# Optimization experiments

Measured on AMD Instinct MI355X. Metric: run time of the kernel, lower is better.

## Reference

```python
import jax, jax.numpy as jnp
import numpy as np
import math

FS = 44100.0
HOP = 256
N_BANDS = 24
KS_BUF = 768  # > max delay 44100/60 = 735 samples


def _lpc1(x, a):
    # order-1 all-pole (sample_wise_lpc with order 1, per-batch constant coeff):
    # y[n] = x[n] - a*y[n-1];  x: [B,N], a: [B]
    def step(yp, xt):
        y = xt - a * yp
        return y, y
    _, ys = jax.lax.scan(step, jnp.zeros_like(a), x.T)
    return ys.T


def _diff_ks(f0_frames, exc, l_b):
    # differentiable Karplus-Strong: fractional-delay loop + 2-tap damping filter.
    # f0_frames: [B,F] Hz, exc: [B,N], l_b: [B,F,2] (loop_coeff, loop_mix logits)
    B, N = exc.shape
    g = 0.999 * jax.nn.sigmoid(l_b[..., 0])   # loop gain in (0, 0.999)
    s = jax.nn.sigmoid(l_b[..., 1])           # loop-filter mix
    up = lambda p: jnp.repeat(p, HOP, axis=1)[:, :N]
    g_s, s_s = up(g), up(s)
    f0_s = up(jnp.clip(f0_frames, 60.0, None))
    D = jnp.clip(FS / f0_s, 2.0, 735.0)        # delay in samples
    Di = jnp.floor(D).astype(jnp.int32)
    fr = (D - Di).astype(exc.dtype)
    L = KS_BUF

    def step(carry, xs):
        buf, n = carry                         # buf: [B,L] circular delay line
        x_t, Di_t, fr_t, g_t, s_t = xs         # each [B]
        i1 = jnp.mod(n - Di_t, L)
        i2 = jnp.mod(n - Di_t - 1, L)
        i3 = jnp.mod(n - Di_t - 2, L)
        take = lambda i: jnp.take_along_axis(buf, i[:, None], axis=1)[:, 0]
        b1, b2, b3 = take(i1), take(i2), take(i3)
        z = (1.0 - fr_t) * b1 + fr_t * b2      # fractional-delay read y[n-D]
        z1 = (1.0 - fr_t) * b2 + fr_t * b3     # y[n-D-1]
        y = x_t + g_t * ((1.0 - s_t) * z + s_t * z1)
        buf = buf.at[:, jnp.mod(n, L)].set(y)
        return (buf, n + 1), y

    xs = (exc.T, Di.T, fr.T, g_s.T, s_s.T)
    init = (jnp.zeros((B, L), exc.dtype), jnp.int32(0))
    _, ys = jax.lax.scan(step, init, xs)
    return ys.T


def _body(x, body_gains):
    # bank of 24 two-pole resonators, log-spaced 80..8000 Hz, Q=10
    fc = jnp.geomspace(80.0, 8000.0, N_BANDS).astype(x.dtype)
    w = 2.0 * jnp.pi * fc / FS
    r = jnp.exp(-jnp.pi * fc / (10.0 * FS))
    a1 = -2.0 * r * jnp.cos(w)
    a2 = r * r
    b0 = 1.0 - r
    B = x.shape[0]

    def step(carry, xt):
        y1, y2 = carry                          # [B,24] each
        y = b0 * xt[:, None] - a1 * y1 - a2 * y2
        return (y, y1), jnp.sum(y * body_gains, axis=-1)

    init = (jnp.zeros((B, N_BANDS), x.dtype), jnp.zeros((B, N_BANDS), x.dtype))
    _, out = jax.lax.scan(step, init, x.T)
    return out.T


def _forward(excitation, pitch, w1, b1, w2, b2, excitation_gain, body_gains):
    B, _, N = excitation.shape
    h = jax.nn.relu(pitch @ w1.T + b1)
    mlp_out = h @ w2.T + b2                     # [B,3]
    loop_coeff = jnp.clip(mlp_out[:, 0], -2.0, 2.5)
    loop_mix = jnp.clip(mlp_out[:, 1], -2.5, 0.0)
    frames = N // HOP
    l_b = jnp.broadcast_to(jnp.stack([loop_coeff, loop_mix], -1)[:, None, :], (B, frames, 2))
    f0_frames = jnp.broadcast_to(pitch, (B, frames))
    exc_sq = (excitation * excitation_gain)[:, 0, :]
    f0_hz = jnp.clip(pitch[:, 0], 60.0, None)
    mult = jnp.clip(2.0 + 6.0 * (f0_hz - 60.0) / 600.0, 2.0, 8.0)
    cutoff = jnp.minimum(2.0 * jnp.pi * f0_hz * mult / FS, jnp.pi * 0.9)
    alpha = 1.0 - jnp.exp(-cutoff)
    exc_f = _lpc1(exc_sq * alpha[:, None], alpha - 1.0)   # pre-KS one-pole LP
    string = _diff_ks(f0_frames, exc_f, l_b)
    loop_post = jnp.clip(mlp_out[:, 2], -4.0, 4.0)
    cutoff_post = jnp.minimum(jnp.pi * jax.nn.sigmoid(loop_post), jnp.pi * 0.99)
    alpha_p = 1.0 - jnp.exp(-cutoff_post)
    string = _lpc1(string * alpha_p[:, None], alpha_p - 1.0)  # post one-pole LP
    out = _body(string, body_gains)
    return out[:, None, :], loop_coeff.mean(), loop_mix.mean(), loop_post.mean()


def setup_inputs():
    key = jax.random.key(0)
    k = jax.random.split(key, 6)
    B, N = 8, 32768
    excitation = jax.random.normal(k[0], (B, 1, N), dtype=jnp.float32)
    pitch = 60.0 + 600.0 * jax.random.uniform(k[1], (B, 1), dtype=jnp.float32)
    bnd1 = 0.1 * math.sqrt(6.0 / (1 + 16))   # xavier_uniform, gain 0.1
    bnd2 = 0.1 * math.sqrt(6.0 / (16 + 3))
    w1 = jax.random.uniform(k[2], (16, 1), jnp.float32, -bnd1, bnd1)
    b1 = jnp.zeros((16,), jnp.float32)
    w2 = jax.random.uniform(k[3], (3, 16), jnp.float32, -bnd2, bnd2)
    b2 = jnp.array([0.9, 0.0, 0.0], jnp.float32)
    excitation_gain = jnp.array(0.25, jnp.float32)
    body_gains = 0.006 * jnp.ones((1, N_BANDS), jnp.float32)
    return {"excitation": excitation, "pitch": pitch, "w1": w1, "b1": b1,
            "w2": w2, "b2": b2, "excitation_gain": excitation_gain,
            "body_gains": body_gains}


def reference(excitation, pitch, w1, b1, w2, b2, excitation_gain, body_gains):
    return _forward(excitation, pitch, w1, b1, w2, b2, excitation_gain, body_gains)
```

## Files before the change

### kernel.cpp

```cpp
#include <hip/hip_runtime.h>
#include <math.h>

#define NSAMP 32768
#define FS_F 44100.0f
#define PI_F 3.14159265358979323846f
#define T1 1024
#define FLAG_MAGIC 0x5A5A5A5A

#define XCAP 33536
#define LWS_OFF 33536
#define TABS_OFF 33568
#define SMEM_FLOATS 40480

struct BParams {
  float alpha, alpha_p;
  float fr, g, s;
  int Di;
  float lc, lm, lp;
};

__device__ inline float sigmoidf_(float x) { return 1.0f / (1.0f + expf(-x)); }

__device__ inline BParams compute_params(int b, const float* __restrict__ pitch,
                                         const float* __restrict__ w1,
                                         const float* __restrict__ b1,
                                         const float* __restrict__ w2,
                                         const float* __restrict__ b2) {
  BParams P;
  float p = pitch[b];
  float h[16];
#pragma unroll
  for (int i = 0; i < 16; ++i) {
    float v = fmaf(p, w1[i], b1[i]);
    h[i] = v > 0.0f ? v : 0.0f;
  }
  float m[3];
#pragma unroll
  for (int j = 0; j < 3; ++j) {
    float acc = b2[j];
#pragma unroll
    for (int i = 0; i < 16; ++i) acc = fmaf(h[i], w2[j * 16 + i], acc);
    m[j] = acc;
  }
  P.lc = fminf(fmaxf(m[0], -2.0f), 2.5f);
  P.lm = fminf(fmaxf(m[1], -2.5f), 0.0f);
  P.lp = fminf(fmaxf(m[2], -4.0f), 4.0f);
  P.g = 0.999f * sigmoidf_(P.lc);
  P.s = sigmoidf_(P.lm);
  float f0 = fmaxf(p, 60.0f);
  float D = fminf(fmaxf(FS_F / f0, 2.0f), 735.0f);
  int Di = (int)floorf(D);
  P.fr = D - (float)Di;
  P.Di = Di;
  float mult = fminf(fmaxf(2.0f + 6.0f * (f0 - 60.0f) / 600.0f, 2.0f), 8.0f);
  float cutoff = fminf(2.0f * PI_F * f0 * mult / FS_F, PI_F * 0.9f);
  P.alpha = 1.0f - expf(-cutoff);
  float cpost = fminf(PI_F * sigmoidf_(P.lp), PI_F * 0.99f);
  P.alpha_p = 1.0f - expf(-cpost);
  return P;
}

__device__ inline float rlv(float v, int l) {
  return __int_as_float(__builtin_amdgcn_readlane(__float_as_int(v), l));
}
__device__ inline float shr1(float v, float bnd) {
  return __int_as_float(__builtin_amdgcn_update_dpp(
      __float_as_int(bnd), __float_as_int(v), 0x138 , 0xf, 0xf,
      false));
}
__device__ inline float ror1(float v) {
  return __int_as_float(__builtin_amdgcn_update_dpp(
      __float_as_int(v), __float_as_int(v), 0x13C , 0xf, 0xf,
      false));
}

__device__ inline void band_coef(int k, float& a1, float& a2, float& b0) {
  float fc = 80.0f * exp2f((float)k * (6.64385618977472436f / 23.0f));
  float w = 2.0f * PI_F * fc / FS_F;
  float r = expf(-PI_F * fc / (10.0f * FS_F));
  a1 = -2.0f * r * cosf(w);
  a2 = r * r;
  b0 = 1.0f - r;
}

__device__ inline void gen_tables(float* __restrict__ tabs, int W) {
  if (W >= 120) return;
  const int j = W / 5, sub = W % 5;
  float A1, A2, B0;
  band_coef(j, A1, A2, B0);
  if (sub == 0) *(float4*)&tabs[j * 4] = make_float4(A1, A2, B0, 0.f);
  float Q00 = -A1, Q01 = -A2, Q10 = 1.f, Q11 = 0.f;
#pragma unroll
  for (int sq = 0; sq < 2; ++sq) {
    float n00 = fmaf(Q00, Q00, Q01 * Q10);
    float n01 = fmaf(Q00, Q01, Q01 * Q11);
    float n10 = fmaf(Q10, Q00, Q11 * Q10);
    float n11 = fmaf(Q10, Q01, Q11 * Q11);
    Q00 = n00; Q01 = n01; Q10 = n10; Q11 = n11;
  }
  float K00 = Q00, K01 = Q01, K10 = Q10, K11 = Q11;
#pragma unroll
  for (int sq = 0; sq < 2; ++sq) {
    float n00 = fmaf(Q00, Q00, Q01 * Q10);
    float n01 = fmaf(Q00, Q01, Q01 * Q11);
    float n10 = fmaf(Q10, Q00, Q11 * Q10);
    float n11 = fmaf(Q10, Q01, Q11 * Q11);
    Q00 = n00; Q01 = n01; Q10 = n10; Q11 = n11;
  }
  float L00[7], L01[7], L10[7], L11[7];
  L00[0] = fmaf(Q00, K00, Q01 * K10);
  L01[0] = fmaf(Q00, K01, Q01 * K11);
  L10[0] = fmaf(Q10, K00, Q11 * K10);
  L11[0] = fmaf(Q10, K01, Q11 * K11);
#pragma unroll
  for (int k = 0; k < 6; ++k) {
    float s00 = fmaf(L00[k], L00[k], L01[k] * L10[k]);
    float s01 = fmaf(L00[k], L01[k], L01[k] * L11[k]);
    float s10 = fmaf(L10[k], L00[k], L11[k] * L10[k]);
    float s11 = fmaf(L10[k], L01[k], L11[k] * L11[k]);
    L00[k + 1] = s00; L01[k + 1] = s01; L10[k + 1] = s10; L11[k + 1] = s11;
  }
  if (sub == 0) {
#pragma unroll
    for (int k = 0; k < 6; ++k)
      *(float4*)&tabs[96 + (k * 24 + j) * 4] =
          make_float4(L00[k], L01[k], L10[k], L11[k]);
    *(float4*)&tabs[672 + j * 4] = make_float4(L00[6], L01[6], L10[6], L11[6]);
  }
  int l0 = sub * 13, l1 = l0 + 13;
  if (l1 > 64) l1 = 64;
  for (int l = l0; l < l1; ++l) {
    float R00 = 1.f, R01 = 0.f, R10 = 0.f, R11 = 1.f;
#pragma unroll
    for (int bit = 0; bit < 6; ++bit) {
      if ((l >> bit) & 1) {
        float n00 = fmaf(L00[bit], R00, L01[bit] * R10);
        float n01 = fmaf(L00[bit], R01, L01[bit] * R11);
        float n10 = fmaf(L10[bit], R00, L11[bit] * R10);
        float n11 = fmaf(L10[bit], R01, L11[bit] * R11);
        R00 = n00; R01 = n01; R10 = n10; R11 = n11;
      }
    }
    *(float4*)&tabs[768 + (j * 64 + l) * 4] = make_float4(R00, R01, R10, R11);
  }
}

template <int KNUM>
__device__ void ks_wave0(float* __restrict__ yg, const float* xall, int lane,
                         int C, float c0w, float c1w, float c2w, int s1,
                         int n0, int end, int span) {
  const int lq1 = (C - 1) - (KNUM - 1) * 64;
  const int W = n0 - s1;
  float yp[KNUM], xC[KNUM], xN[KNUM];
  float p1 = 0.f, p2 = 0.f;
#pragma unroll
  for (int k = 0; k < KNUM; ++k) {
    yp[k] = 0.f;
    xC[k] = xall[lane + (k << 6)];
    xN[k] = xall[C + lane + (k << 6)];
  }
  int rel = 0;
  while (rel + C <= W) {
    float b2v[KNUM], b3v[KNUM];
    b2v[0] = shr1(yp[0], p1);
#pragma unroll
    for (int k = 1; k < KNUM; ++k) b2v[k] = shr1(yp[k], ror1(yp[k - 1]));
    b3v[0] = shr1(b2v[0], p2);
#pragma unroll
    for (int k = 1; k < KNUM; ++k) b3v[k] = shr1(b2v[k], ror1(b2v[k - 1]));
    float p1n = rlv(yp[KNUM - 1], lq1);
    float p2n = rlv(b2v[KNUM - 1], lq1);
#pragma unroll
    for (int k = 0; k < KNUM; ++k)
      yp[k] = fmaf(c0w, yp[k], fmaf(c2w, b3v[k], fmaf(c1w, b2v[k], xC[k])));
    p1 = p1n;
    p2 = p2n;
    int r2 = rel + 2 * C;
    if (r2 < span) {
      const float* xp = &xall[r2 + lane];
#pragma unroll
      for (int k = 0; k < KNUM; ++k) {
        xC[k] = xN[k];
        xN[k] = xp[k << 6];
      }
    } else {
#pragma unroll
      for (int k = 0; k < KNUM; ++k) xC[k] = xN[k];
    }
    rel += C;
  }
  while (rel < span) {
    float b2v[KNUM], b3v[KNUM];
    b2v[0] = shr1(yp[0], p1);
#pragma unroll
    for (int k = 1; k < KNUM; ++k) b2v[k] = shr1(yp[k], ror1(yp[k - 1]));
    b3v[0] = shr1(b2v[0], p2);
#pragma unroll
    for (int k = 1; k < KNUM; ++k) b3v[k] = shr1(b2v[k], ror1(b2v[k - 1]));
    float p1n = rlv(yp[KNUM - 1], lq1);
    float p2n = rlv(b2v[KNUM - 1], lq1);
#pragma unroll
    for (int k = 0; k < KNUM; ++k)
      yp[k] = fmaf(c0w, yp[k], fmaf(c2w, b3v[k], fmaf(c1w, b2v[k], xC[k])));
    p1 = p1n;
    p2 = p2n;
#pragma unroll
    for (int k = 0; k < KNUM; ++k) {
      int i = lane + (k << 6);
      int n = s1 + rel + i;
      bool okl = (k < KNUM - 1) || (lane <= lq1);
      if (okl && n >= n0 && n < end) yg[n] = yp[k];
    }
    int r2 = rel + 2 * C;
    if (r2 < span) {
      const float* xp = &xall[r2 + lane];
#pragma unroll
      for (int k = 0; k < KNUM; ++k) {
        xC[k] = xN[k];
        xN[k] = xp[k << 6];
      }
    } else {
#pragma unroll
      for (int k = 0; k < KNUM; ++k) xC[k] = xN[k];
    }
    rel += C;
  }
}

__device__ inline void ks_phase(int b, int q, const BParams& P,
                                const float* __restrict__ exc, float scale0,
                                float* __restrict__ buf1, float* xall,
                                float* lws, float* tabs, int t) {
  const int C = P.Di;
  const int n0 = q << 10;
  float lg = -logf(P.g);
  int Wp = (int)ceilf(10.5f / fmaxf(lg, 1e-6f));
  if (Wp > 64) Wp = 64;
  if (Wp < 4) Wp = 4;
  int W = Wp * C;
  if (W > n0) W = n0;
  W = (W + 3) & ~3;
  const int s1 = n0 - W;
  const int span = W + T1;
  const int end = n0 + T1;
  const int NSG = (span + 2047) >> 11;
  float* yg = buf1 + (size_t)b * NSAMP;
  const float* xg = exc + (size_t)b * NSAMP;

  const float c = 1.0f - P.alpha;
  const float scale = scale0 * P.alpha;
  const float c2v = c * c, c4 = c2v * c2v, c8 = c4 * c4, c16 = c8 * c8;
  const float c32 = c16 * c16, c64 = c32 * c32, c128 = c64 * c64;
  const float c256 = c128 * c128, c512 = c256 * c256, c1024 = c512 * c512;
  const float c2048 = c1024 * c1024;
  const int lane = t & 63, wid = t >> 6;
  const float c32lane = exp2f((float)(lane << 5) * log2f(c));

  for (int r = 0; r < 5; ++r) {
    int si = r * 4 + wid;
    if (si > NSG) break;
    int sg = si - 1;
    int gbase = s1 + (sg << 11) + (lane << 5);
    float4 pf[8];
#pragma unroll
    for (int i = 0; i < 8; ++i) {
      int g = gbase + 4 * i;
      float4 v = make_float4(0.f, 0.f, 0.f, 0.f);
      if (g >= 0 && g + 3 < NSAMP) v = *(const float4*)&xg[g];
      pf[i] = v;
    }
    float S = 0.0f;
#pragma unroll
    for (int i = 0; i < 8; ++i) {
      S = fmaf(c, S, scale * pf[i].x);
      S = fmaf(c, S, scale * pf[i].y);
      S = fmaf(c, S, scale * pf[i].z);
      S = fmaf(c, S, scale * pf[i].w);
    }
    float Sw = S, u;
    u = __shfl_up(Sw, 1);  if (lane >= 1)  Sw = fmaf(c32, u, Sw);
    u = __shfl_up(Sw, 2);  if (lane >= 2)  Sw = fmaf(c64, u, Sw);
    u = __shfl_up(Sw, 4);  if (lane >= 4)  Sw = fmaf(c128, u, Sw);
    u = __shfl_up(Sw, 8);  if (lane >= 8)  Sw = fmaf(c256, u, Sw);
    u = __shfl_up(Sw, 16); if (lane >= 16) Sw = fmaf(c512, u, Sw);
    u = __shfl_up(Sw, 32); if (lane >= 32) Sw = fmaf(c1024, u, Sw);
    float tot = rlv(Sw, 63);
    float Sex = __shfl_up(Sw, 1);
    if (lane == 0) Sex = 0.0f;
    if (lane == 0) lws[si] = tot;
    if (sg >= 0) {
      float v = Sex;
#pragma unroll
      for (int i = 0; i < 8; ++i) {
        float4 y;
        v = fmaf(c, v, scale * pf[i].x); y.x = v;
        v = fmaf(c, v, scale * pf[i].y); y.y = v;
        v = fmaf(c, v, scale * pf[i].z); y.z = v;
        v = fmaf(c, v, scale * pf[i].w); y.w = v;
        pf[i] = y;
      }
      int o = (sg << 11) + (lane << 5);
#pragma unroll
      for (int i = 0; i < 8; ++i) {
        int ci = (lane + i) & 7;
        *(float4*)&xall[o + 4 * ci] = pf[ci];
      }
    }
  }
  if (4 * t < 768) {
    *(float4*)&xall[(NSG << 11) + 4 * t] = make_float4(0.f, 0.f, 0.f, 0.f);
  }
  __syncthreads();
  {
    float p4[8];
    p4[0] = 1.0f;
#pragma unroll
    for (int i = 1; i < 8; ++i) p4[i] = p4[i - 1] * c4;
    for (int r = 0; r < 5; ++r) {
      int si = r * 4 + wid;
      if (si > NSG) break;
      int sg = si - 1;
      if (sg < 0) continue;
      float vr = 0.0f;
      for (int i = 0; i < si; ++i) vr = fmaf(c2048, vr, lws[i]);
      float corr0 = c * (c32lane * vr);
      int o = (sg << 11) + (lane << 5);
#pragma unroll
      for (int i = 0; i < 8; ++i) {
        int ci = (lane + i) & 7;
        float4 y = *(float4*)&xall[o + 4 * ci];
        float f = corr0 * p4[ci];
        y.x += f; f *= c;
        y.y += f; f *= c;
        y.z += f; f *= c;
        y.w += f;
        *(float4*)&xall[o + 4 * ci] = y;
      }
    }
  }
  __syncthreads();

  const float c0w = P.g * (1.0f - P.s) * (1.0f - P.fr);
  const float c1w = P.g * ((1.0f - P.s) * P.fr + P.s * (1.0f - P.fr));
  const float c2w = P.g * P.s * P.fr;
  if (wid == 0) {
    switch ((C + 63) >> 6) {
      case 2:  ks_wave0<2>(yg, xall, lane, C, c0w, c1w, c2w, s1, n0, end, span); break;
      case 3:  ks_wave0<3>(yg, xall, lane, C, c0w, c1w, c2w, s1, n0, end, span); break;
      case 4:  ks_wave0<4>(yg, xall, lane, C, c0w, c1w, c2w, s1, n0, end, span); break;
      case 5:  ks_wave0<5>(yg, xall, lane, C, c0w, c1w, c2w, s1, n0, end, span); break;
      case 6:  ks_wave0<6>(yg, xall, lane, C, c0w, c1w, c2w, s1, n0, end, span); break;
      case 7:  ks_wave0<7>(yg, xall, lane, C, c0w, c1w, c2w, s1, n0, end, span); break;
      case 8:  ks_wave0<8>(yg, xall, lane, C, c0w, c1w, c2w, s1, n0, end, span); break;
      case 9:  ks_wave0<9>(yg, xall, lane, C, c0w, c1w, c2w, s1, n0, end, span); break;
      case 10: ks_wave0<10>(yg, xall, lane, C, c0w, c1w, c2w, s1, n0, end, span); break;
      case 11: ks_wave0<11>(yg, xall, lane, C, c0w, c1w, c2w, s1, n0, end, span); break;
      default: ks_wave0<12>(yg, xall, lane, C, c0w, c1w, c2w, s1, n0, end, span); break;
    }
  } else if (wid >= 2) {
    gen_tables(tabs, (wid - 2) * 64 + lane);
  }
}

__device__ inline void lpc_lds(const float* __restrict__ xg,
                               float* __restrict__ sl, int s2, int nt, int lim,
                               float scale, float c, int t, float* lws) {
  const int lane = t & 63, wid = t >> 6;
  float c2v = c * c, c4 = c2v * c2v, c8 = c4 * c4;
  float m1 = c8, m2 = m1 * m1, m4 = m2 * m2, m8 = m4 * m4, m16 = m8 * m8,
        m32 = m16 * m16;
  float c512 = m32 * m32;
  float c2048 = c512 * c512;
  c2048 *= c2048;
  float l2c = log2f(c);
  float c8lane = exp2f((float)(8 * lane) * l2c);
  float cgk = exp2f((float)(8 * t) * l2c);
  float vrun = 0.0f;
  for (int tile = 0; tile < nt; ++tile) {
    __syncthreads();
    int g0 = s2 + (tile << 11) + 8 * t;
    float4 xa = make_float4(0.f, 0.f, 0.f, 0.f);
    float4 xb = make_float4(0.f, 0.f, 0.f, 0.f);
    if (g0 + 3 < lim) xa = *(const float4*)&xg[g0];
    if (g0 + 7 < lim) xb = *(const float4*)&xg[g0 + 4];
    float S = 0.0f;
    S = fmaf(c, S, scale * xa.x); S = fmaf(c, S, scale * xa.y);
    S = fmaf(c, S, scale * xa.z); S = fmaf(c, S, scale * xa.w);
    S = fmaf(c, S, scale * xb.x); S = fmaf(c, S, scale * xb.y);
    S = fmaf(c, S, scale * xb.z); S = fmaf(c, S, scale * xb.w);
    float Sw = S, u;
    u = __shfl_up(Sw, 1);  if (lane >= 1)  Sw = fmaf(m1, u, Sw);
    u = __shfl_up(Sw, 2);  if (lane >= 2)  Sw = fmaf(m2, u, Sw);
    u = __shfl_up(Sw, 4);  if (lane >= 4)  Sw = fmaf(m4, u, Sw);
    u = __shfl_up(Sw, 8);  if (lane >= 8)  Sw = fmaf(m8, u, Sw);
    u = __shfl_up(Sw, 16); if (lane >= 16) Sw = fmaf(m16, u, Sw);
    u = __shfl_up(Sw, 32); if (lane >= 32) Sw = fmaf(m32, u, Sw);
    if (lane == 63) lws[wid] = Sw;
    __syncthreads();
    float a0 = lws[0], a1w = lws[1], a2w = lws[2], a3w = lws[3];
    float carry = (wid == 1)   ? a0
                  : (wid == 2) ? fmaf(c512, a0, a1w)
                  : (wid == 3) ? fmaf(c512, fmaf(c512, a0, a1w), a2w)
                               : 0.0f;
    float Sprev = __shfl_up(Sw, 1);
    float Sex = (lane == 0) ? 0.0f : Sprev;
    Sex = fmaf(c8lane, carry, Sex);
    float v = fmaf(cgk, vrun, Sex);
    int o = g0 - s2;
    float4 ya, yb;
    v = fmaf(c, v, scale * xa.x); ya.x = v;
    v = fmaf(c, v, scale * xa.y); ya.y = v;
    v = fmaf(c, v, scale * xa.z); ya.z = v;
    v = fmaf(c, v, scale * xa.w); ya.w = v;
    v = fmaf(c, v, scale * xb.x); yb.x = v;
    v = fmaf(c, v, scale * xb.y); yb.y = v;
    v = fmaf(c, v, scale * xb.z); yb.z = v;
    v = fmaf(c, v, scale * xb.w); yb.w = v;
    *(float4*)&sl[o] = ya;
    *(float4*)&sl[o + 4] = yb;
    float tS = fmaf(c512, fmaf(c512, fmaf(c512, a0, a1w), a2w), a3w);
    vrun = fmaf(c2048, vrun, tS);
  }
}

__device__ inline void body_phase(int b, int q, const BParams& P,
                                  const float* __restrict__ gains,
                                  const float* __restrict__ buf1,
                                  float* __restrict__ out, float* sl,
                                  float* lws, float (*lc0)[8],
                                  float (*lc1)[8], const float* tabs, int t) {
  const int lane = t & 63, wid = t >> 6;
  const int n0 = q << 10;
  const int base = n0 - 4096;
  int s2 = base - 256;
  if (s2 < 0) s2 = 0;
  const int end = n0 + 1024;
  const int nt = (end - s2 + 2047) >> 11;

  lpc_lds(buf1 + (size_t)b * NSAMP, sl, s2, nt, end, P.alpha_p,
          1.0f - P.alpha_p, t, lws);
  __syncthreads();

  const float* bandcL = tabs;
  const float* QlevL = tabs + 96;
  const float* QwL = tabs + 672;
  const float* RtabL = tabs + 768;

  const int tb = base + 20 * t;
  float4 acc[5];
#pragma unroll
  for (int i = 0; i < 5; ++i) acc[i] = make_float4(0.f, 0.f, 0.f, 0.f);

  for (int g = 0; g < 3; ++g) {
    float A1[8], A2[8], B0[8], GN[8];
#pragma unroll
    for (int j = 0; j < 8; ++j) {
      int k = g * 8 + j;
      float4 bc = *(const float4*)&bandcL[k * 4];
      A1[j] = bc.x; A2[j] = bc.y; B0[j] = bc.z;
      GN[j] = gains[k];
    }
    float cv0[8], cv1[8];
#pragma unroll
    for (int j = 0; j < 8; ++j) cv0[j] = cv1[j] = 0.f;
    for (int i = 0; i < 5; ++i) {
      int n = tb + 4 * i;
      float4 xv = make_float4(0.f, 0.f, 0.f, 0.f);
      if (n >= 0) xv = *(const float4*)&sl[n - s2];
#pragma unroll
      for (int e = 0; e < 4; ++e) {
        float xi = e == 0 ? xv.x : e == 1 ? xv.y : e == 2 ? xv.z : xv.w;
#pragma unroll
        for (int j = 0; j < 8; ++j) {
          float nc = fmaf(B0[j], xi, -fmaf(A1[j], cv0[j], A2[j] * cv1[j]));
          cv1[j] = cv0[j];
          cv0[j] = nc;
        }
      }
    }
    int kl = 0;
    for (int off = 1; off <= 32; off <<= 1, ++kl) {
      float q00[8], q01[8], q10[8], q11[8];
#pragma unroll
      for (int j = 0; j < 8; ++j) {
        float4 qv = *(const float4*)&QlevL[(kl * 24 + g * 8 + j) * 4];
        q00[j] = qv.x; q01[j] = qv.y; q10[j] = qv.z; q11[j] = qv.w;
      }
#pragma unroll
      for (int j = 0; j < 8; ++j) {
        float u0 = __shfl_up(cv0[j], off);
        float u1 = __shfl_up(cv1[j], off);
        if (lane >= off) {
          float nc0 = fmaf(q00[j], u0, fmaf(q01[j], u1, cv0[j]));
          float nc1 = fmaf(q10[j], u0, fmaf(q11[j], u1, cv1[j]));
          cv0[j] = nc0;
          cv1[j] = nc1;
        }
      }
    }
    __syncthreads();
    if (lane == 63) {
#pragma unroll
      for (int j = 0; j < 8; ++j) {
        lc0[wid][j] = cv0[j];
        lc1[wid][j] = cv1[j];
      }
    }
    __syncthreads();
    float qw00[8], qw01[8], qw10[8], qw11[8];
#pragma unroll
    for (int j = 0; j < 8; ++j) {
      float4 qv = *(const float4*)&QwL[(g * 8 + j) * 4];
      qw00[j] = qv.x; qw01[j] = qv.y; qw10[j] = qv.z; qw11[j] = qv.w;
    }
    float car0[8], car1[8];
#pragma unroll
    for (int j = 0; j < 8; ++j) car0[j] = car1[j] = 0.f;
    for (int v = 0; v < wid; ++v) {
#pragma unroll
      for (int j = 0; j < 8; ++j) {
        float n0c = fmaf(qw00[j], car0[j], fmaf(qw01[j], car1[j], lc0[v][j]));
        float n1c = fmaf(qw10[j], car0[j], fmaf(qw11[j], car1[j], lc1[v][j]));
        car0[j] = n0c;
        car1[j] = n1c;
      }
    }
    float y1[8], y2[8];
#pragma unroll
    for (int j = 0; j < 8; ++j) {
      float4 rv = *(const float4*)&RtabL[((g * 8 + j) * 64 + lane) * 4];
      float e0 = __shfl_up(cv0[j], 1);
      float e1 = __shfl_up(cv1[j], 1);
      if (lane == 0) { e0 = 0.f; e1 = 0.f; }
      y1[j] = fmaf(rv.x, car0[j], fmaf(rv.y, car1[j], e0));
      y2[j] = fmaf(rv.z, car0[j], fmaf(rv.w, car1[j], e1));
    }
    if (tb + 20 > n0) {
      for (int i = 0; i < 5; ++i) {
        float4 xv = *(const float4*)&sl[tb - s2 + 4 * i];
        float4 ov = acc[i];
#pragma unroll
        for (int e = 0; e < 4; ++e) {
          float xi = e == 0 ? xv.x : e == 1 ? xv.y : e == 2 ? xv.z : xv.w;
          float a = 0.f;
#pragma unroll
          for (int j = 0; j < 8; ++j) {
            float yv = fmaf(B0[j], xi, -fmaf(A1[j], y1[j], A2[j] * y2[j]));
            y2[j] = y1[j];
            y1[j] = yv;
            a = fmaf(GN[j], yv, a);
          }
          if (e == 0) ov.x += a;
          else if (e == 1) ov.y += a;
          else if (e == 2) ov.z += a;
          else ov.w += a;
        }
        acc[i] = ov;
      }
    }
  }
  if (tb + 20 > n0) {
    float* outb = out + (size_t)b * NSAMP;
#pragma unroll
    for (int i = 0; i < 5; ++i) {
      int n = tb + 4 * i;
      if (n >= n0) *(float4*)&outb[n] = acc[i];
    }
  }
}

__global__ void __launch_bounds__(256, 1) synth_all(
    const float* __restrict__ exc, const float* __restrict__ pitch,
    const float* __restrict__ w1, const float* __restrict__ b1,
    const float* __restrict__ w2, const float* __restrict__ b2,
    const float* __restrict__ eg, const float* __restrict__ gains,
    float* __restrict__ buf1, int* __restrict__ flags,
    float* __restrict__ out) {
  extern __shared__ float smem[];
  const int blk = blockIdx.x;
  const int b = blk >> 5, q = blk & 31;
  const int t = threadIdx.x;

  BParams P = compute_params(b, pitch, w1, b1, w2, b2);
  if (blk == 0 && t < 64) {
    int bb = (t < 8) ? t : 0;
    BParams Q = compute_params(bb, pitch, w1, b1, w2, b2);
    float slc = 0.f, slm = 0.f, slp = 0.f;
    for (int i = 0; i < 8; ++i) {
      slc += rlv(Q.lc, i);
      slm += rlv(Q.lm, i);
      slp += rlv(Q.lp, i);
    }
    if (t == 0) {
      out[8 * NSAMP + 0] = slc / 8.0f;
      out[8 * NSAMP + 1] = slm / 8.0f;
      out[8 * NSAMP + 2] = slp / 8.0f;
    }
  }

  ks_phase(b, q, P, exc, eg[0], buf1, smem, smem + LWS_OFF, smem + TABS_OFF, t);
  __syncthreads();

  const int n0 = q << 10;
  int s2 = n0 - 4096 - 256;
  if (s2 < 0) s2 = 0;
  const int qlo = s2 >> 10;
  if (t == 0) {
    __hip_atomic_store(&flags[blk], FLAG_MAGIC, __ATOMIC_RELEASE,
                       __HIP_MEMORY_SCOPE_AGENT);
    for (int f = qlo; f < q; ++f) {
      while (__hip_atomic_load(&flags[b * 32 + f], __ATOMIC_ACQUIRE,
                               __HIP_MEMORY_SCOPE_AGENT) != FLAG_MAGIC) {
        __builtin_amdgcn_s_sleep(8);
      }
    }
  }
  __syncthreads();

  body_phase(b, q, P, gains, buf1, out, smem, smem + 6144,
             (float(*)[8])(smem + 6152), (float(*)[8])(smem + 6184),
             smem + TABS_OFF, t);
}

extern "C" void kernel_launch(void* const* d_in, const int* in_sizes, int n_in,
                              void* d_out, int out_size, void* d_ws, size_t ws_size,
                              hipStream_t stream) {
  const float* exc = (const float*)d_in[0];
  const float* pitch = (const float*)d_in[1];
  const float* w1 = (const float*)d_in[2];
  const float* b1 = (const float*)d_in[3];
  const float* w2 = (const float*)d_in[4];
  const float* b2 = (const float*)d_in[5];
  const float* eg = (const float*)d_in[6];
  const float* bg = (const float*)d_in[7];
  float* out = (float*)d_out;
  float* buf1 = (float*)d_ws;
  int* flags = (int*)(buf1 + 8 * NSAMP);

  static int lds_set = 0;
  if (!lds_set) {
    hipFuncSetAttribute(reinterpret_cast<const void*>(synth_all),
                        hipFuncAttributeMaxDynamicSharedMemorySize,
                        SMEM_FLOATS * 4);
    lds_set = 1;
  }
  hipLaunchKernelGGL(synth_all, dim3(256), dim3(256), SMEM_FLOATS * 4, stream,
                     exc, pitch, w1, b1, w2, b2, eg, bg, buf1, flags, out);
}
```

Baseline: 126.7 us.

## Restructure excitation prefilter scan into block-wide per-segment scan with prefetch

Replaces the two-pass segment scan (each wave scans a 2048-sample segment with 32 samples per lane, then a second pass applies carry corrections) with a sequential loop over segments. In that loop all 256 threads cooperatively scan each segment at 8 samples per thread, combine wave totals through LDS and carry a running value, so no correction pass is needed. Global loads for the next segment are double-buffered in registers. The trade is two barriers per segment and a serialized segment loop, in exchange for dropping the second LDS read-modify-write pass and cutting per-thread serial work.

```diff
diff --git a/kernel.cpp b/kernel.cpp
--- a/kernel.cpp
+++ b/kernel.cpp
@@ -74,6 +74,10 @@
       false));
 }
 
+__device__ inline void barrier_lgkm() {
+  asm volatile("s_waitcnt lgkmcnt(0)\n\ts_barrier" ::: "memory");
+}
+
 __device__ inline void band_coef(int k, float& a1, float& a2, float& b0) {
   float fc = 80.0f * exp2f((float)k * (6.64385618977472436f / 23.0f));
   float w = 2.0f * PI_F * fc / FS_F;
@@ -143,6 +147,67 @@
     }
     *(float4*)&tabs[768 + (j * 64 + l) * 4] = make_float4(R00, R01, R10, R11);
   }
+}
+
+struct SCtx {
+  float scale, c;
+  float m1, m2, m4, m8, m16, m32, c512, c2048, c8lane, cgk;
+  float vrun;
+  float* lws;
+};
+
+__device__ inline void ld2(const float* __restrict__ p, int g0, float4& a,
+                           float4& b) {
+  a = make_float4(0.f, 0.f, 0.f, 0.f);
+  b = make_float4(0.f, 0.f, 0.f, 0.f);
+  if (g0 >= 0 && g0 + 3 < NSAMP) a = *(const float4*)&p[g0];
+  if (g0 + 4 >= 0 && g0 + 7 < NSAMP) b = *(const float4*)&p[g0 + 4];
+}
+
+__device__ inline void scan_seg_flat(SCtx& SC, float* xall, int sg, bool write,
+                                     int t, float4 xa, float4 xb) {
+  const int lane = t & 63, wid = t >> 6;
+  barrier_lgkm();
+  const float c = SC.c, scale = SC.scale;
+  float S = 0.0f;
+  S = fmaf(c, S, scale * xa.x); S = fmaf(c, S, scale * xa.y);
+  S = fmaf(c, S, scale * xa.z); S = fmaf(c, S, scale * xa.w);
+  S = fmaf(c, S, scale * xb.x); S = fmaf(c, S, scale * xb.y);
+  S = fmaf(c, S, scale * xb.z); S = fmaf(c, S, scale * xb.w);
+  float Sw = S, u;
+  u = __shfl_up(Sw, 1);  if (lane >= 1)  Sw = fmaf(SC.m1, u, Sw);
+  u = __shfl_up(Sw, 2);  if (lane >= 2)  Sw = fmaf(SC.m2, u, Sw);
+  u = __shfl_up(Sw, 4);  if (lane >= 4)  Sw = fmaf(SC.m4, u, Sw);
+  u = __shfl_up(Sw, 8);  if (lane >= 8)  Sw = fmaf(SC.m8, u, Sw);
+  u = __shfl_up(Sw, 16); if (lane >= 16) Sw = fmaf(SC.m16, u, Sw);
+  u = __shfl_up(Sw, 32); if (lane >= 32) Sw = fmaf(SC.m32, u, Sw);
+  if (lane == 63) SC.lws[wid] = Sw;
+  barrier_lgkm();
+  float a0 = SC.lws[0], a1w = SC.lws[1], a2w = SC.lws[2], a3w = SC.lws[3];
+  float carry = (wid == 1)   ? a0
+                : (wid == 2) ? fmaf(SC.c512, a0, a1w)
+                : (wid == 3) ? fmaf(SC.c512, fmaf(SC.c512, a0, a1w), a2w)
+                             : 0.0f;
+  float Sprev = __shfl_up(Sw, 1);
+  float Sex = (lane == 0) ? 0.0f : Sprev;
+  Sex = fmaf(SC.c8lane, carry, Sex);
+  float v = fmaf(SC.cgk, SC.vrun, Sex);
+  float4 ya, yb;
+  v = fmaf(c, v, scale * xa.x); ya.x = v;
+  v = fmaf(c, v, scale * xa.y); ya.y = v;
+  v = fmaf(c, v, scale * xa.z); ya.z = v;
+  v = fmaf(c, v, scale * xa.w); ya.w = v;
+  v = fmaf(c, v, scale * xb.x); yb.x = v;
+  v = fmaf(c, v, scale * xb.y); yb.y = v;
+  v = fmaf(c, v, scale * xb.z); yb.z = v;
+  v = fmaf(c, v, scale * xb.w); yb.w = v;
+  if (write) {
+    int o = (sg << 11) + 8 * t;
+    *(float4*)&xall[o] = ya;
+    *(float4*)&xall[o + 4] = yb;
+  }
+  float tS = fmaf(SC.c512, fmaf(SC.c512, fmaf(SC.c512, a0, a1w), a2w), a3w);
+  SC.vrun = fmaf(SC.c2048, SC.vrun, tS);
 }
 
 template <int KNUM>
@@ -247,102 +312,47 @@
   float* yg = buf1 + (size_t)b * NSAMP;
   const float* xg = exc + (size_t)b * NSAMP;
 
-  const float c = 1.0f - P.alpha;
-  const float scale = scale0 * P.alpha;
-  const float c2v = c * c, c4 = c2v * c2v, c8 = c4 * c4, c16 = c8 * c8;
-  const float c32 = c16 * c16, c64 = c32 * c32, c128 = c64 * c64;
-  const float c256 = c128 * c128, c512 = c256 * c256, c1024 = c512 * c512;
-  const float c2048 = c1024 * c1024;
-  const int lane = t & 63, wid = t >> 6;
-  const float c32lane = exp2f((float)(lane << 5) * log2f(c));
-
-  for (int r = 0; r < 5; ++r) {
-    int si = r * 4 + wid;
-    if (si > NSG) break;
-    int sg = si - 1;
-    int gbase = s1 + (sg << 11) + (lane << 5);
-    float4 pf[8];
-#pragma unroll
-    for (int i = 0; i < 8; ++i) {
-      int g = gbase + 4 * i;
-      float4 v = make_float4(0.f, 0.f, 0.f, 0.f);
-      if (g >= 0 && g + 3 < NSAMP) v = *(const float4*)&xg[g];
-      pf[i] = v;
-    }
-    float S = 0.0f;
-#pragma unroll
-    for (int i = 0; i < 8; ++i) {
-      S = fmaf(c, S, scale * pf[i].x);
-      S = fmaf(c, S, scale * pf[i].y);
-      S = fmaf(c, S, scale * pf[i].z);
-      S = fmaf(c, S, scale * pf[i].w);
-    }
-    float Sw = S, u;
-    u = __shfl_up(Sw, 1);  if (lane >= 1)  Sw = fmaf(c32, u, Sw);
-    u = __shfl_up(Sw, 2);  if (lane >= 2)  Sw = fmaf(c64, u, Sw);
-    u = __shfl_up(Sw, 4);  if (lane >= 4)  Sw = fmaf(c128, u, Sw);
-    u = __shfl_up(Sw, 8);  if (lane >= 8)  Sw = fmaf(c256, u, Sw);
-    u = __shfl_up(Sw, 16); if (lane >= 16) Sw = fmaf(c512, u, Sw);
-    u = __shfl_up(Sw, 32); if (lane >= 32) Sw = fmaf(c1024, u, Sw);
-    float tot = rlv(Sw, 63);
-    float Sex = __shfl_up(Sw, 1);
-    if (lane == 0) Sex = 0.0f;
-    if (lane == 0) lws[si] = tot;
-    if (sg >= 0) {
-      float v = Sex;
-#pragma unroll
-      for (int i = 0; i < 8; ++i) {
-        float4 y;
-        v = fmaf(c, v, scale * pf[i].x); y.x = v;
-        v = fmaf(c, v, scale * pf[i].y); y.y = v;
-        v = fmaf(c, v, scale * pf[i].z); y.z = v;
-        v = fmaf(c, v, scale * pf[i].w); y.w = v;
-        pf[i] = y;
-      }
-      int o = (sg << 11) + (lane << 5);
-#pragma unroll
-      for (int i = 0; i < 8; ++i) {
-        int ci = (lane + i) & 7;
-        *(float4*)&xall[o + 4 * ci] = pf[ci];
-      }
-    }
+  SCtx SC;
+  SC.c = 1.0f - P.alpha;
+  SC.scale = scale0 * P.alpha;
+  {
+    float c = SC.c;
+    float c2v = c * c, c4 = c2v * c2v, c8 = c4 * c4;
+    SC.m1 = c8;
+    SC.m2 = SC.m1 * SC.m1;
+    SC.m4 = SC.m2 * SC.m2;
+    SC.m8 = SC.m4 * SC.m4;
+    SC.m16 = SC.m8 * SC.m8;
+    SC.m32 = SC.m16 * SC.m16;
+    SC.c512 = SC.m32 * SC.m32;
+    float c1024 = SC.c512 * SC.c512;
+    SC.c2048 = c1024 * c1024;
+    float l2c = log2f(c);
+    SC.c8lane = exp2f((float)(8 * (t & 63)) * l2c);
+    SC.cgk = exp2f((float)(8 * t) * l2c);
+  }
+  SC.vrun = 0.0f;
+  SC.lws = lws;
+
+  float4 xa, xb, na, nb;
+  float4 ta = make_float4(0.f, 0.f, 0.f, 0.f);
+  float4 tb = make_float4(0.f, 0.f, 0.f, 0.f);
+  ld2(xg, s1 - 2048 + 8 * t, xa, xb);
+  ld2(xg, s1 + 8 * t, na, nb);
+  for (int si = 0; si <= NSG; ++si) {
+    if (si + 2 <= NSG) ld2(xg, s1 + ((si + 1) << 11) + 8 * t, ta, tb);
+    scan_seg_flat(SC, xall, si - 1, si > 0, t, xa, xb);
+    xa = na; xb = nb; na = ta; nb = tb;
   }
   if (4 * t < 768) {
     *(float4*)&xall[(NSG << 11) + 4 * t] = make_float4(0.f, 0.f, 0.f, 0.f);
-  }
-  __syncthreads();
-  {
-    float p4[8];
-    p4[0] = 1.0f;
-#pragma unroll
-    for (int i = 1; i < 8; ++i) p4[i] = p4[i - 1] * c4;
-    for (int r = 0; r < 5; ++r) {
-      int si = r * 4 + wid;
-      if (si > NSG) break;
-      int sg = si - 1;
-      if (sg < 0) continue;
-      float vr = 0.0f;
-      for (int i = 0; i < si; ++i) vr = fmaf(c2048, vr, lws[i]);
-      float corr0 = c * (c32lane * vr);
-      int o = (sg << 11) + (lane << 5);
-#pragma unroll
-      for (int i = 0; i < 8; ++i) {
-        int ci = (lane + i) & 7;
-        float4 y = *(float4*)&xall[o + 4 * ci];
-        float f = corr0 * p4[ci];
-        y.x += f; f *= c;
-        y.y += f; f *= c;
-        y.z += f; f *= c;
-        y.w += f;
-        *(float4*)&xall[o + 4 * ci] = y;
-      }
-    }
   }
   __syncthreads();
 
   const float c0w = P.g * (1.0f - P.s) * (1.0f - P.fr);
   const float c1w = P.g * ((1.0f - P.s) * P.fr + P.s * (1.0f - P.fr));
   const float c2w = P.g * P.s * P.fr;
+  const int lane = t & 63, wid = t >> 6;
   if (wid == 0) {
     switch ((C + 63) >> 6) {
       case 2:  ks_wave0<2>(yg, xall, lane, C, c0w, c1w, c2w, s1, n0, end, span); break;
```

Measured after the change: 110.7 us. 1.14x faster.

## Pipeline excitation LPC prefilter in wave 1 with KS recurrence via progress flag

Applied to the files above, without the earlier changes.

The block-parallel LPC prefilter of the excitation, which used all four waves, two block barriers and a separate correction pass, is replaced. One wave now computes the prefilter segment by segment with a running carry and double-buffered global loads, and publishes progress through an LDS atomic counter. The Karplus-Strong wave polls that counter and starts consuming segments while later ones are still being produced. This removes the barriers and the correction pass and overlaps the prefilter with the serial recurrence, at the cost of serialising the prefilter onto a single wave and adding spin-wait polling.

```diff
diff --git a/kernel.cpp b/kernel.cpp
--- a/kernel.cpp
+++ b/kernel.cpp
@@ -7,10 +7,10 @@
 #define T1 1024
 #define FLAG_MAGIC 0x5A5A5A5A
 
-#define XCAP 33536
-#define LWS_OFF 33536
-#define TABS_OFF 33568
-#define SMEM_FLOATS 40480
+#define XALL_FLOATS 33792
+#define PROG_OFF 33792
+#define TABS_OFF 33808
+#define SMEM_FLOATS 40720
 
 struct BParams {
   float alpha, alpha_p;
@@ -145,92 +145,119 @@
   }
 }
 
+__device__ inline void w1_load(const float* __restrict__ xg, int s1, int seg,
+                               int lane, float4* pf) {
+  const int base = s1 + (seg << 11) + (lane << 5);
+#pragma unroll
+  for (int i = 0; i < 8; ++i) {
+    const int g = base + 4 * i;
+    float4 v = make_float4(0.f, 0.f, 0.f, 0.f);
+    if (g >= 0 && g + 3 < NSAMP) v = *(const float4*)&xg[g];
+    pf[i] = v;
+  }
+}
+
 template <int KNUM>
-__device__ void ks_wave0(float* __restrict__ yg, const float* xall, int lane,
-                         int C, float c0w, float c1w, float c2w, int s1,
-                         int n0, int end, int span) {
+__device__ void ks_wave0(float* __restrict__ yg, const float* xall,
+                         int* __restrict__ prog, int lane, int C, float c0w,
+                         float c1w, float c2w, int s1, int n0, int end,
+                         int span, int NSG) {
   const int lq1 = (C - 1) - (KNUM - 1) * 64;
   const int W = n0 - s1;
   float yp[KNUM], xC[KNUM], xN[KNUM];
   float p1 = 0.f, p2 = 0.f;
-#pragma unroll
-  for (int k = 0; k < KNUM; ++k) {
-    yp[k] = 0.f;
-    xC[k] = xall[lane + (k << 6)];
-    xN[k] = xall[C + lane + (k << 6)];
-  }
   int rel = 0;
-  while (rel + C <= W) {
-    float b2v[KNUM], b3v[KNUM];
-    b2v[0] = shr1(yp[0], p1);
-#pragma unroll
-    for (int k = 1; k < KNUM; ++k) b2v[k] = shr1(yp[k], ror1(yp[k - 1]));
-    b3v[0] = shr1(b2v[0], p2);
-#pragma unroll
-    for (int k = 1; k < KNUM; ++k) b3v[k] = shr1(b2v[k], ror1(b2v[k - 1]));
-    float p1n = rlv(yp[KNUM - 1], lq1);
-    float p2n = rlv(b2v[KNUM - 1], lq1);
-#pragma unroll
-    for (int k = 0; k < KNUM; ++k)
-      yp[k] = fmaf(c0w, yp[k], fmaf(c2w, b3v[k], fmaf(c1w, b2v[k], xC[k])));
-    p1 = p1n;
-    p2 = p2n;
-    int r2 = rel + 2 * C;
-    if (r2 < span) {
-      const float* xp = &xall[r2 + lane];
+#pragma unroll
+  for (int k = 0; k < KNUM; ++k) { yp[k] = 0.f; xC[k] = 0.f; xN[k] = 0.f; }
+  for (int s = 0; s < NSG; ++s) {
+    int need = s + 3;
+    if (need > NSG) need = NSG;
+    while (__hip_atomic_load(prog, __ATOMIC_ACQUIRE,
+                             __HIP_MEMORY_SCOPE_WORKGROUP) < need) {
+      __builtin_amdgcn_s_sleep(1);
+    }
+    if (s == 0) {
 #pragma unroll
       for (int k = 0; k < KNUM; ++k) {
-        xC[k] = xN[k];
-        xN[k] = xp[k << 6];
-      }
-    } else {
-#pragma unroll
-      for (int k = 0; k < KNUM; ++k) xC[k] = xN[k];
-    }
-    rel += C;
-  }
-  while (rel < span) {
-    float b2v[KNUM], b3v[KNUM];
-    b2v[0] = shr1(yp[0], p1);
-#pragma unroll
-    for (int k = 1; k < KNUM; ++k) b2v[k] = shr1(yp[k], ror1(yp[k - 1]));
-    b3v[0] = shr1(b2v[0], p2);
-#pragma unroll
-    for (int k = 1; k < KNUM; ++k) b3v[k] = shr1(b2v[k], ror1(b2v[k - 1]));
-    float p1n = rlv(yp[KNUM - 1], lq1);
-    float p2n = rlv(b2v[KNUM - 1], lq1);
-#pragma unroll
-    for (int k = 0; k < KNUM; ++k)
-      yp[k] = fmaf(c0w, yp[k], fmaf(c2w, b3v[k], fmaf(c1w, b2v[k], xC[k])));
-    p1 = p1n;
-    p2 = p2n;
-#pragma unroll
-    for (int k = 0; k < KNUM; ++k) {
-      int i = lane + (k << 6);
-      int n = s1 + rel + i;
-      bool okl = (k < KNUM - 1) || (lane <= lq1);
-      if (okl && n >= n0 && n < end) yg[n] = yp[k];
-    }
-    int r2 = rel + 2 * C;
-    if (r2 < span) {
-      const float* xp = &xall[r2 + lane];
+        int i = lane + (k << 6);
+        xC[k] = xall[i];
+        xN[k] = xall[C + i];
+      }
+    }
+    int fence = (s + 1) << 11;
+    if (fence > span) fence = span;
+    while (rel + C <= W && rel < fence) {
+      float b2v[KNUM], b3v[KNUM];
+      b2v[0] = shr1(yp[0], p1);
+#pragma unroll
+      for (int k = 1; k < KNUM; ++k) b2v[k] = shr1(yp[k], ror1(yp[k - 1]));
+      b3v[0] = shr1(b2v[0], p2);
+#pragma unroll
+      for (int k = 1; k < KNUM; ++k) b3v[k] = shr1(b2v[k], ror1(b2v[k - 1]));
+      float p1n = rlv(yp[KNUM - 1], lq1);
+      float p2n = rlv(b2v[KNUM - 1], lq1);
+#pragma unroll
+      for (int k = 0; k < KNUM; ++k)
+        yp[k] = fmaf(c0w, yp[k], fmaf(c2w, b3v[k], fmaf(c1w, b2v[k], xC[k])));
+      p1 = p1n;
+      p2 = p2n;
+      int r2 = rel + 2 * C;
+      if (r2 < span) {
+        const float* xp = &xall[r2 + lane];
+#pragma unroll
+        for (int k = 0; k < KNUM; ++k) {
+          xC[k] = xN[k];
+          xN[k] = xp[k << 6];
+        }
+      } else {
+#pragma unroll
+        for (int k = 0; k < KNUM; ++k) xC[k] = xN[k];
+      }
+      rel += C;
+    }
+    while (rel < fence) {
+      float b2v[KNUM], b3v[KNUM];
+      b2v[0] = shr1(yp[0], p1);
+#pragma unroll
+      for (int k = 1; k < KNUM; ++k) b2v[k] = shr1(yp[k], ror1(yp[k - 1]));
+      b3v[0] = shr1(b2v[0], p2);
+#pragma unroll
+      for (int k = 1; k < KNUM; ++k) b3v[k] = shr1(b2v[k], ror1(b2v[k - 1]));
+      float p1n = rlv(yp[KNUM - 1], lq1);
+      float p2n = rlv(b2v[KNUM - 1], lq1);
+#pragma unroll
+      for (int k = 0; k < KNUM; ++k)
+        yp[k] = fmaf(c0w, yp[k], fmaf(c2w, b3v[k], fmaf(c1w, b2v[k], xC[k])));
+      p1 = p1n;
+      p2 = p2n;
 #pragma unroll
       for (int k = 0; k < KNUM; ++k) {
-        xC[k] = xN[k];
-        xN[k] = xp[k << 6];
-      }
-    } else {
-#pragma unroll
-      for (int k = 0; k < KNUM; ++k) xC[k] = xN[k];
-    }
-    rel += C;
+        int i = lane + (k << 6);
+        int n = s1 + rel + i;
+        bool okl = (k < KNUM - 1) || (lane <= lq1);
+        if (okl && n >= n0 && n < end) yg[n] = yp[k];
+      }
+      int r2 = rel + 2 * C;
+      if (r2 < span) {
+        const float* xp = &xall[r2 + lane];
+#pragma unroll
+        for (int k = 0; k < KNUM; ++k) {
+          xC[k] = xN[k];
+          xN[k] = xp[k << 6];
+        }
+      } else {
+#pragma unroll
+        for (int k = 0; k < KNUM; ++k) xC[k] = xN[k];
+      }
+      rel += C;
+    }
   }
 }
 
 __device__ inline void ks_phase(int b, int q, const BParams& P,
                                 const float* __restrict__ exc, float scale0,
                                 float* __restrict__ buf1, float* xall,
-                                float* lws, float* tabs, int t) {
+                                int* prog, float* tabs, int t) {
   const int C = P.Di;
   const int n0 = q << 10;
   float lg = -logf(P.g);
@@ -249,115 +276,86 @@
 
   const float c = 1.0f - P.alpha;
   const float scale = scale0 * P.alpha;
-  const float c2v = c * c, c4 = c2v * c2v, c8 = c4 * c4, c16 = c8 * c8;
-  const float c32 = c16 * c16, c64 = c32 * c32, c128 = c64 * c64;
-  const float c256 = c128 * c128, c512 = c256 * c256, c1024 = c512 * c512;
-  const float c2048 = c1024 * c1024;
   const int lane = t & 63, wid = t >> 6;
-  const float c32lane = exp2f((float)(lane << 5) * log2f(c));
-
-  for (int r = 0; r < 5; ++r) {
-    int si = r * 4 + wid;
-    if (si > NSG) break;
-    int sg = si - 1;
-    int gbase = s1 + (sg << 11) + (lane << 5);
-    float4 pf[8];
-#pragma unroll
-    for (int i = 0; i < 8; ++i) {
-      int g = gbase + 4 * i;
-      float4 v = make_float4(0.f, 0.f, 0.f, 0.f);
-      if (g >= 0 && g + 3 < NSAMP) v = *(const float4*)&xg[g];
-      pf[i] = v;
-    }
-    float S = 0.0f;
-#pragma unroll
-    for (int i = 0; i < 8; ++i) {
-      S = fmaf(c, S, scale * pf[i].x);
-      S = fmaf(c, S, scale * pf[i].y);
-      S = fmaf(c, S, scale * pf[i].z);
-      S = fmaf(c, S, scale * pf[i].w);
-    }
-    float Sw = S, u;
-    u = __shfl_up(Sw, 1);  if (lane >= 1)  Sw = fmaf(c32, u, Sw);
-    u = __shfl_up(Sw, 2);  if (lane >= 2)  Sw = fmaf(c64, u, Sw);
-    u = __shfl_up(Sw, 4);  if (lane >= 4)  Sw = fmaf(c128, u, Sw);
-    u = __shfl_up(Sw, 8);  if (lane >= 8)  Sw = fmaf(c256, u, Sw);
-    u = __shfl_up(Sw, 16); if (lane >= 16) Sw = fmaf(c512, u, Sw);
-    u = __shfl_up(Sw, 32); if (lane >= 32) Sw = fmaf(c1024, u, Sw);
-    float tot = rlv(Sw, 63);
-    float Sex = __shfl_up(Sw, 1);
-    if (lane == 0) Sex = 0.0f;
-    if (lane == 0) lws[si] = tot;
-    if (sg >= 0) {
-      float v = Sex;
-#pragma unroll
-      for (int i = 0; i < 8; ++i) {
-        float4 y;
-        v = fmaf(c, v, scale * pf[i].x); y.x = v;
-        v = fmaf(c, v, scale * pf[i].y); y.y = v;
-        v = fmaf(c, v, scale * pf[i].z); y.z = v;
-        v = fmaf(c, v, scale * pf[i].w); y.w = v;
-        pf[i] = y;
-      }
-      int o = (sg << 11) + (lane << 5);
-#pragma unroll
-      for (int i = 0; i < 8; ++i) {
-        int ci = (lane + i) & 7;
-        *(float4*)&xall[o + 4 * ci] = pf[ci];
-      }
-    }
-  }
-  if (4 * t < 768) {
-    *(float4*)&xall[(NSG << 11) + 4 * t] = make_float4(0.f, 0.f, 0.f, 0.f);
-  }
-  __syncthreads();
-  {
-    float p4[8];
-    p4[0] = 1.0f;
-#pragma unroll
-    for (int i = 1; i < 8; ++i) p4[i] = p4[i - 1] * c4;
-    for (int r = 0; r < 5; ++r) {
-      int si = r * 4 + wid;
-      if (si > NSG) break;
-      int sg = si - 1;
-      if (sg < 0) continue;
-      float vr = 0.0f;
-      for (int i = 0; i < si; ++i) vr = fmaf(c2048, vr, lws[i]);
-      float corr0 = c * (c32lane * vr);
-      int o = (sg << 11) + (lane << 5);
-#pragma unroll
-      for (int i = 0; i < 8; ++i) {
-        int ci = (lane + i) & 7;
-        float4 y = *(float4*)&xall[o + 4 * ci];
-        float f = corr0 * p4[ci];
-        y.x += f; f *= c;
-        y.y += f; f *= c;
-        y.z += f; f *= c;
-        y.w += f;
-        *(float4*)&xall[o + 4 * ci] = y;
-      }
-    }
-  }
+
+  if (t == 0) *prog = 0;
+  *(float4*)&xall[(NSG << 11) + 4 * t] = make_float4(0.f, 0.f, 0.f, 0.f);
   __syncthreads();
 
   const float c0w = P.g * (1.0f - P.s) * (1.0f - P.fr);
   const float c1w = P.g * ((1.0f - P.s) * P.fr + P.s * (1.0f - P.fr));
   const float c2w = P.g * P.s * P.fr;
+
   if (wid == 0) {
     switch ((C + 63) >> 6) {
-      case 2:  ks_wave0<2>(yg, xall, lane, C, c0w, c1w, c2w, s1, n0, end, span); break;
-      case 3:  ks_wave0<3>(yg, xall, lane, C, c0w, c1w, c2w, s1, n0, end, span); break;
-      case 4:  ks_wave0<4>(yg, xall, lane, C, c0w, c1w, c2w, s1, n0, end, span); break;
-      case 5:  ks_wave0<5>(yg, xall, lane, C, c0w, c1w, c2w, s1, n0, end, span); break;
-      case 6:  ks_wave0<6>(yg, xall, lane, C, c0w, c1w, c2w, s1, n0, end, span); break;
-      case 7:  ks_wave0<7>(yg, xall, lane, C, c0w, c1w, c2w, s1, n0, end, span); break;
-      case 8:  ks_wave0<8>(yg, xall, lane, C, c0w, c1w, c2w, s1, n0, end, span); break;
-      case 9:  ks_wave0<9>(yg, xall, lane, C, c0w, c1w, c2w, s1, n0, end, span); break;
-      case 10: ks_wave0<10>(yg, xall, lane, C, c0w, c1w, c2w, s1, n0, end, span); break;
-      case 11: ks_wave0<11>(yg, xall, lane, C, c0w, c1w, c2w, s1, n0, end, span); break;
-      default: ks_wave0<12>(yg, xall, lane, C, c0w, c1w, c2w, s1, n0, end, span); break;
-    }
-  } else if (wid >= 2) {
+      case 2:  ks_wave0<2>(yg, xall, prog, lane, C, c0w, c1w, c2w, s1, n0, end, span, NSG); break;
+      case 3:  ks_wave0<3>(yg, xall, prog, lane, C, c0w, c1w, c2w, s1, n0, end, span, NSG); break;
+      case 4:  ks_wave0<4>(yg, xall, prog, lane, C, c0w, c1w, c2w, s1, n0, end, span, NSG); break;
+      case 5:  ks_wave0<5>(yg, xall, prog, lane, C, c0w, c1w, c2w, s1, n0, end, span, NSG); break;
+      case 6:  ks_wave0<6>(yg, xall, prog, lane, C, c0w, c1w, c2w, s1, n0, end, span, NSG); break;
+      case 7:  ks_wave0<7>(yg, xall, prog, lane, C, c0w, c1w, c2w, s1, n0, end, span, NSG); break;
+      case 8:  ks_wave0<8>(yg, xall, prog, lane, C, c0w, c1w, c2w, s1, n0, end, span, NSG); break;
+      case 9:  ks_wave0<9>(yg, xall, prog, lane, C, c0w, c1w, c2w, s1, n0, end, span, NSG); break;
+      case 10: ks_wave0<10>(yg, xall, prog, lane, C, c0w, c1w, c2w, s1, n0, end, span, NSG); break;
+      case 11: ks_wave0<11>(yg, xall, prog, lane, C, c0w, c1w, c2w, s1, n0, end, span, NSG); break;
+      default: ks_wave0<12>(yg, xall, prog, lane, C, c0w, c1w, c2w, s1, n0, end, span, NSG); break;
+    }
+  } else if (wid == 1) {
+    float c2v = c * c, c4 = c2v * c2v, c8 = c4 * c4;
+    float m1 = c8, m2 = m1 * m1, m4 = m2 * m2, m8 = m4 * m4, m16 = m8 * m8,
+          m32 = m16 * m16;
+    float c512 = m32 * m32;
+    float c1024 = c512 * c512;
+    float c2048 = c1024 * c1024;
+    const float n1 = m4, n2 = m8, n4 = m16, n8 = m32, n16 = c512,
+                n32 = c512 * c512;
+    const float c32lane = exp2f((float)(lane << 5) * log2f(c));
+    float vrun = 0.0f;
+    float4 pf[8], pg[8];
+    w1_load(xg, s1, -1, lane, pf);
+    w1_load(xg, s1, 0, lane, pg);
+    for (int ls = -1; ls < NSG; ++ls) {
+      float S = 0.0f;
+#pragma unroll
+      for (int i = 0; i < 8; ++i) {
+        S = fmaf(c, S, scale * pf[i].x);
+        S = fmaf(c, S, scale * pf[i].y);
+        S = fmaf(c, S, scale * pf[i].z);
+        S = fmaf(c, S, scale * pf[i].w);
+      }
+      float Sw = S, u;
+      u = __shfl_up(Sw, 1);  if (lane >= 1)  Sw = fmaf(n1, u, Sw);
+      u = __shfl_up(Sw, 2);  if (lane >= 2)  Sw = fmaf(n2, u, Sw);
+      u = __shfl_up(Sw, 4);  if (lane >= 4)  Sw = fmaf(n4, u, Sw);
+      u = __shfl_up(Sw, 8);  if (lane >= 8)  Sw = fmaf(n8, u, Sw);
+      u = __shfl_up(Sw, 16); if (lane >= 16) Sw = fmaf(n16, u, Sw);
+      u = __shfl_up(Sw, 32); if (lane >= 32) Sw = fmaf(n32, u, Sw);
+      float tot = rlv(Sw, 63);
+      float Sex = __shfl_up(Sw, 1);
+      if (lane == 0) Sex = 0.0f;
+      if (ls >= 0) {
+        float v = fmaf(c32lane, vrun, Sex);
+        const int o = (ls << 11) + (lane << 5);
+#pragma unroll
+        for (int i = 0; i < 8; ++i) {
+          float4 y;
+          v = fmaf(c, v, scale * pf[i].x); y.x = v;
+          v = fmaf(c, v, scale * pf[i].y); y.y = v;
+          v = fmaf(c, v, scale * pf[i].z); y.z = v;
+          v = fmaf(c, v, scale * pf[i].w); y.w = v;
+          *(float4*)&xall[o + 4 * i] = y;
+        }
+      }
+      vrun = fmaf(c2048, vrun, tot);
+      if (ls >= 0 && lane == 0) {
+        __hip_atomic_store(prog, ls + 1, __ATOMIC_RELEASE,
+                           __HIP_MEMORY_SCOPE_WORKGROUP);
+      }
+#pragma unroll
+      for (int i = 0; i < 8; ++i) pf[i] = pg[i];
+      if (ls + 2 < NSG) w1_load(xg, s1, ls + 2, lane, pg);
+    }
+  } else {
     gen_tables(tabs, (wid - 2) * 64 + lane);
   }
 }
@@ -598,7 +596,8 @@
     }
   }
 
-  ks_phase(b, q, P, exc, eg[0], buf1, smem, smem + LWS_OFF, smem + TABS_OFF, t);
+  ks_phase(b, q, P, exc, eg[0], buf1, smem, (int*)&smem[PROG_OFF],
+           smem + TABS_OFF, t);
   __syncthreads();
 
   const int n0 = q << 10;
```

New measurement: 113.9 us. -10.1%, faster.
